# Optimization experiments

Hardware: AMD Instinct MI355X
Metric: run time of the kernel (lower is better)

The kernel has to match this reference:

```python
import jax, jax.numpy as jnp
import numpy as np
from jax import lax

C = 320
GN_GROUPS = 32
EPS = 1e-5


def setup_inputs() -> dict:
    key = jax.random.key(0)
    ks = jax.random.split(key, 5)
    x = jax.random.normal(ks[0], (16, C, 96, 96), dtype=jnp.float32)
    # depthwise 3x3 kernel [C,1,3,3] (OIHW with feature_group_count=C)
    dw_w = jax.random.normal(ks[1], (C, 1, 3, 3), dtype=jnp.float32) * 0.1
    dw_b = jax.random.normal(ks[2], (C,), dtype=jnp.float32) * 0.01
    gn_w = jnp.ones((C,), dtype=jnp.float32)
    gn_b = jnp.zeros((C,), dtype=jnp.float32)
    proj_w = jax.random.normal(ks[3], (C,), dtype=jnp.float32) * 0.001
    proj_b = jnp.full((1,), -4.0, dtype=jnp.float32)
    return {"x": x, "dw_w": dw_w, "dw_b": dw_b, "gn_w": gn_w,
            "gn_b": gn_b, "proj_w": proj_w, "proj_b": proj_b}


def _group_norm(h, gamma, beta):
    # h: [B,C,H,W]; GN over (C//G, H, W) within each of G groups; biased var (torch)
    B, Cc, H, W = h.shape
    hg = h.reshape(B, GN_GROUPS, Cc // GN_GROUPS, H, W)
    mean = jnp.mean(hg, axis=(2, 3, 4), keepdims=True)
    var = jnp.mean(jnp.square(hg - mean), axis=(2, 3, 4), keepdims=True)
    hn = ((hg - mean) * lax.rsqrt(var + EPS)).reshape(B, Cc, H, W)
    return hn * gamma[None, :, None, None] + beta[None, :, None, None]


def reference(x, dw_w, dw_b, gn_w, gn_b, proj_w, proj_b):
    # depthwise 3x3 conv, padding=1
    h = lax.conv_general_dilated(
        x, dw_w, window_strides=(1, 1), padding=((1, 1), (1, 1)),
        dimension_numbers=("NCHW", "OIHW", "NCHW"), feature_group_count=C)
    h = h + dw_b[None, :, None, None]
    h = _group_norm(h, gn_w, gn_b)
    # 1x1 conv C -> 1 == per-pixel channel dot product
    g = jnp.einsum("bchw,c->bhw", h, proj_w) + proj_b[0]
    return jax.nn.sigmoid(g)[:, None, :, :]  # [B,1,H,W]
```

## Files before the change

kernel.cpp:

```cpp
#include <hip/hip_runtime.h>
#include <math.h>

#define HH 96
#define WW 96
#define NPIX (HH*WW)
#define CC 320
#define GG 32
#define CPG 10
#define YT 6
#define TR 16
#define TPB 512

__global__ __launch_bounds__(TPB)
void k_main(const float* __restrict__ x, const float* __restrict__ dw_w,
            const float* __restrict__ dw_b, const float* __restrict__ gn_w,
            const float* __restrict__ proj_w,
            float* __restrict__ P, float* __restrict__ partials) {
  const int bid = blockIdx.x;
  const int yt = bid % YT;
  const int t  = bid / YT;
  const int gr = t & 31;
  const int b  = t >> 5;

  __shared__ float wsm[CPG * 9], ssm[CPG], bsm[CPG];
  const int tid = threadIdx.x;
  if (tid < CPG * 9) wsm[tid] = dw_w[gr * CPG * 9 + tid];
  if (tid < CPG) {
    int c = gr * CPG + tid;
    ssm[tid] = proj_w[c] * gn_w[c];
    bsm[tid] = dw_b[c];
  }
  __syncthreads();

  const int lane = tid & 63;
  const int xcl  = tid & 31;
  const int r    = tid >> 5;
  const bool active = xcl < 24;
  const float mact  = active ? 1.f : 0.f;
  const int xc  = min(xcl, 23);
  const int Y   = yt * TR + r;

  const float mtop = (Y > 0)      ? 1.f : 0.f;
  const float mbot = (Y < HH - 1) ? 1.f : 0.f;
  const int ytop = max(Y - 1, 0);
  const int ybot = min(Y + 1, HH - 1);
  const float mlft = (xcl > 0)  ? 1.f : 0.f;
  const float mrgt = (xcl < 23) ? 1.f : 0.f;
  const int lm1 = (lane >= 1)  ? lane - 1 : lane;
  const int lp1 = (lane <= 62) ? lane + 1 : lane;

  const size_t off_t = (size_t)ytop * WW + xc * 4;
  const size_t off_m = (size_t)Y    * WW + xc * 4;
  const size_t off_b = (size_t)ybot * WW + xc * 4;
  const float* xg = x + ((size_t)(b * CC + gr * CPG)) * NPIX;

  float p0 = 0.f, p1 = 0.f, p2 = 0.f, p3 = 0.f, s1 = 0.f, s2 = 0.f;

  #pragma unroll 1
  for (int cl = 0; cl < CPG; ++cl) {
    const float* img = xg + cl * NPIX;
    float4 vt = *(const float4*)(img + off_t);
    float4 vm = *(const float4*)(img + off_m);
    float4 vb = *(const float4*)(img + off_b);
    vt.x *= mtop; vt.y *= mtop; vt.z *= mtop; vt.w *= mtop;
    vb.x *= mbot; vb.y *= mbot; vb.z *= mbot; vb.w *= mbot;

    float tl = __shfl(vt.w, lm1) * mlft;
    float ml = __shfl(vm.w, lm1) * mlft;
    float bl = __shfl(vb.w, lm1) * mlft;
    float tr_ = __shfl(vt.x, lp1) * mrgt;
    float mr = __shfl(vm.x, lp1) * mrgt;
    float br = __shfl(vb.x, lp1) * mrgt;

    const float* wp = &wsm[cl * 9];
    const float w0 = wp[0], w1 = wp[1], w2 = wp[2];
    const float w3 = wp[3], w4 = wp[4], w5 = wp[5];
    const float w6 = wp[6], w7 = wp[7], w8 = wp[8];

    float u0 = w0*tl   + w1*vt.x + w2*vt.y
             + w3*ml   + w4*vm.x + w5*vm.y
             + w6*bl   + w7*vb.x + w8*vb.y;
    float u1 = w0*vt.x + w1*vt.y + w2*vt.z
             + w3*vm.x + w4*vm.y + w5*vm.z
             + w6*vb.x + w7*vb.y + w8*vb.z;
    float u2 = w0*vt.y + w1*vt.z + w2*vt.w
             + w3*vm.y + w4*vm.z + w5*vm.w
             + w6*vb.y + w7*vb.z + w8*vb.w;
    float u3 = w0*vt.z + w1*vt.w + w2*tr_
             + w3*vm.z + w4*vm.w + w5*mr
             + w6*vb.z + w7*vb.w + w8*br;

    const float sc = ssm[cl], bias = bsm[cl];
    p0 = fmaf(sc, u0, p0);
    p1 = fmaf(sc, u1, p1);
    p2 = fmaf(sc, u2, p2);
    p3 = fmaf(sc, u3, p3);
    float h0 = u0 + bias, h1 = u1 + bias, h2 = u2 + bias, h3 = u3 + bias;
    s1 += mact * ((h0 + h1) + (h2 + h3));
    s2 += mact * (fmaf(h0, h0, h1 * h1) + fmaf(h2, h2, h3 * h3));
  }

  if (active) {
    size_t pidx = ((size_t)(b * GG + gr)) * NPIX + (size_t)Y * WW + xcl * 4;
    *(float4*)&P[pidx] = make_float4(p0, p1, p2, p3);
  }

  #pragma unroll
  for (int off = 32; off; off >>= 1) {
    s1 += __shfl_down(s1, off);
    s2 += __shfl_down(s2, off);
  }
  __shared__ float r1[8], r2[8];
  if ((tid & 63) == 0) { r1[tid >> 6] = s1; r2[tid >> 6] = s2; }
  __syncthreads();
  if (tid == 0) {
    float a = 0.f, q = 0.f;
    #pragma unroll
    for (int i = 0; i < 8; ++i) { a += r1[i]; q += r2[i]; }
    size_t o = (((size_t)(b * GG + gr)) * YT + yt) * 2;
    partials[o]     = a;
    partials[o + 1] = q;
  }
}

__global__ __launch_bounds__(512)
void k_coef(const float* __restrict__ partials, const float* __restrict__ dw_b,
            const float* __restrict__ gn_w, const float* __restrict__ gn_b,
            const float* __restrict__ proj_w, const float* __restrict__ proj_b,
            float* __restrict__ rv, float* __restrict__ D) {
  const int tid = threadIdx.x;
  const int b = tid >> 5, gr = tid & 31;
  float s1 = 0.f, s2 = 0.f;
  #pragma unroll
  for (int t = 0; t < YT; ++t) {
    size_t o = (((size_t)(b * GG + gr)) * YT + t) * 2;
    s1 += partials[o];
    s2 += partials[o + 1];
  }
  const float invN = 1.f / (float)(CPG * NPIX);
  float mean = s1 * invN;
  float var  = s2 * invN - mean * mean;
  float rinv = rsqrtf(var + 1e-5f);
  float K = 0.f, E = 0.f;
  #pragma unroll
  for (int i = 0; i < CPG; ++i) {
    int c = gr * CPG + i;
    float pg = proj_w[c] * gn_w[c];
    K = fmaf(pg, dw_b[c] - mean, K);
    E = fmaf(proj_w[c], gn_b[c], E);
  }
  rv[tid] = rinv;
  float contrib = fmaf(rinv, K, E);
  #pragma unroll
  for (int m = 16; m; m >>= 1) contrib += __shfl_xor(contrib, m, 32);
  if (gr == 0) D[b] = contrib + proj_b[0];
}

__global__ __launch_bounds__(256)
void k_out(const float* __restrict__ P, const float* __restrict__ rv,
           const float* __restrict__ D, float* __restrict__ out) {
  const int b   = blockIdx.x / 9;
  const int blk = blockIdx.x % 9;
  __shared__ float rs[GG];
  __shared__ float Ds;
  if (threadIdx.x < GG) rs[threadIdx.x] = rv[b * GG + threadIdx.x];
  if (threadIdx.x == 0) Ds = D[b];
  __syncthreads();

  const int p = (blk * 256 + threadIdx.x) * 4;
  const float* Pb = P + (size_t)b * GG * NPIX + p;
  float g0 = 0.f, g1 = 0.f, g2 = 0.f, g3 = 0.f;
  #pragma unroll 8
  for (int gr = 0; gr < GG; ++gr) {
    float4 v = *(const float4*)(Pb + (size_t)gr * NPIX);
    float rr = rs[gr];
    g0 = fmaf(rr, v.x, g0);
    g1 = fmaf(rr, v.y, g1);
    g2 = fmaf(rr, v.z, g2);
    g3 = fmaf(rr, v.w, g3);
  }
  const float d = Ds;
  float4 o;
  o.x = 1.f / (1.f + expf(-(g0 + d)));
  o.y = 1.f / (1.f + expf(-(g1 + d)));
  o.z = 1.f / (1.f + expf(-(g2 + d)));
  o.w = 1.f / (1.f + expf(-(g3 + d)));
  *(float4*)&out[(size_t)b * NPIX + p] = o;
}

extern "C" void kernel_launch(void* const* d_in, const int* in_sizes, int n_in,
                              void* d_out, int out_size, void* d_ws, size_t ws_size,
                              hipStream_t stream) {
  const float* x      = (const float*)d_in[0];
  const float* dw_w   = (const float*)d_in[1];
  const float* dw_b   = (const float*)d_in[2];
  const float* gn_w   = (const float*)d_in[3];
  const float* gn_b   = (const float*)d_in[4];
  const float* proj_w = (const float*)d_in[5];
  const float* proj_b = (const float*)d_in[6];
  float* out = (float*)d_out;

  const size_t P_BYTES = (size_t)16 * GG * NPIX * 4;
  float* P        = (float*)d_ws;
  float* partials = (float*)((char*)d_ws + P_BYTES);
  float* rv       = (float*)((char*)d_ws + P_BYTES + 24576);
  float* D        = (float*)((char*)d_ws + P_BYTES + 24576 + 2048);

  hipLaunchKernelGGL(k_main, dim3(16 * GG * YT), dim3(TPB), 0, stream,
                     x, dw_w, dw_b, gn_w, proj_w, P, partials);
  hipLaunchKernelGGL(k_coef, dim3(1), dim3(512), 0, stream,
                     partials, dw_b, gn_w, gn_b, proj_w, proj_b, rv, D);
  hipLaunchKernelGGL(k_out, dim3(16 * 9), dim3(256), 0, stream,
                     P, rv, D, out);
}
```

Measured before the change: 58.36 us.

## Compute two rows per thread with prefetch and fold coef kernel into output kernel

Each thread now computes two output rows, so the four input rows it loads are shared between two stencils and the grid shrinks from 6 to 3 row tiles per group. The next channel's rows are prefetched into registers while the current one is computed. The single-block coefficient kernel is removed; each output block recomputes the group statistics and bias term from the partial sums. This cuts one launch and redundant row loads, at the cost of more registers per thread and some duplicated statistics work in every output block.

New measurement: 52.25 us. -10.5%, faster.

```diff
diff --git a/kernel.cpp b/kernel.cpp
--- a/kernel.cpp
+++ b/kernel.cpp
@@ -7,8 +7,7 @@
 #define CC 320
 #define GG 32
 #define CPG 10
-#define YT 6
-#define TR 16
+#define YT 3
 #define TPB 512
 
 __global__ __launch_bounds__(TPB)
@@ -37,72 +36,87 @@
   const int r    = tid >> 5;
   const bool active = xcl < 24;
   const float mact  = active ? 1.f : 0.f;
-  const int xc  = min(xcl, 23);
-  const int Y   = yt * TR + r;
-
-  const float mtop = (Y > 0)      ? 1.f : 0.f;
-  const float mbot = (Y < HH - 1) ? 1.f : 0.f;
-  const int ytop = max(Y - 1, 0);
-  const int ybot = min(Y + 1, HH - 1);
+  const int xc = min(xcl, 23);
+  const int Y0 = yt * 32 + 2 * r;
+  const int Y1 = Y0 + 1;
+
+  const float ma = (Y0 > 0)      ? 1.f : 0.f;
+  const float md = (Y1 < HH - 1) ? 1.f : 0.f;
+  const int ya = max(Y0 - 1, 0);
+  const int yd = min(Y1 + 1, HH - 1);
   const float mlft = (xcl > 0)  ? 1.f : 0.f;
   const float mrgt = (xcl < 23) ? 1.f : 0.f;
-  const int lm1 = (lane >= 1)  ? lane - 1 : lane;
-  const int lp1 = (lane <= 62) ? lane + 1 : lane;
-
-  const size_t off_t = (size_t)ytop * WW + xc * 4;
-  const size_t off_m = (size_t)Y    * WW + xc * 4;
-  const size_t off_b = (size_t)ybot * WW + xc * 4;
+  const int lm1 = (xcl >= 1) ? lane - 1 : lane;
+  const int lp1 = (xcl < 31) ? lane + 1 : lane;
+
+  const size_t offa = (size_t)ya * WW + xc * 4;
+  const size_t offb = (size_t)Y0 * WW + xc * 4;
+  const size_t offc = (size_t)Y1 * WW + xc * 4;
+  const size_t offd = (size_t)yd * WW + xc * 4;
   const float* xg = x + ((size_t)(b * CC + gr * CPG)) * NPIX;
 
-  float p0 = 0.f, p1 = 0.f, p2 = 0.f, p3 = 0.f, s1 = 0.f, s2 = 0.f;
+  float p0=0.f,p1=0.f,p2=0.f,p3=0.f,p4=0.f,p5=0.f,p6=0.f,p7=0.f;
+  float s1 = 0.f, s2 = 0.f;
+
+  float4 A = *(const float4*)(xg + offa);
+  float4 B = *(const float4*)(xg + offb);
+  float4 C = *(const float4*)(xg + offc);
+  float4 D = *(const float4*)(xg + offd);
 
   #pragma unroll 1
-  for (int cl = 0; cl < CPG; ++cl) {
-    const float* img = xg + cl * NPIX;
-    float4 vt = *(const float4*)(img + off_t);
-    float4 vm = *(const float4*)(img + off_m);
-    float4 vb = *(const float4*)(img + off_b);
-    vt.x *= mtop; vt.y *= mtop; vt.z *= mtop; vt.w *= mtop;
-    vb.x *= mbot; vb.y *= mbot; vb.z *= mbot; vb.w *= mbot;
-
-    float tl = __shfl(vt.w, lm1) * mlft;
-    float ml = __shfl(vm.w, lm1) * mlft;
-    float bl = __shfl(vb.w, lm1) * mlft;
-    float tr_ = __shfl(vt.x, lp1) * mrgt;
-    float mr = __shfl(vm.x, lp1) * mrgt;
-    float br = __shfl(vb.x, lp1) * mrgt;
-
-    const float* wp = &wsm[cl * 9];
+  for (int ch = 0; ch < CPG; ++ch) {
+    const float* nimg = xg + (size_t)min(ch + 1, CPG - 1) * NPIX;
+    float4 nA = *(const float4*)(nimg + offa);
+    float4 nB = *(const float4*)(nimg + offb);
+    float4 nC = *(const float4*)(nimg + offc);
+    float4 nD = *(const float4*)(nimg + offd);
+
+    A.x *= ma; A.y *= ma; A.z *= ma; A.w *= ma;
+    D.x *= md; D.y *= md; D.z *= md; D.w *= md;
+
+    float al = __shfl(A.w, lm1) * mlft;
+    float bl = __shfl(B.w, lm1) * mlft;
+    float cl2 = __shfl(C.w, lm1) * mlft;
+    float dl = __shfl(D.w, lm1) * mlft;
+    float ar = __shfl(A.x, lp1) * mrgt;
+    float br = __shfl(B.x, lp1) * mrgt;
+    float cr = __shfl(C.x, lp1) * mrgt;
+    float dr = __shfl(D.x, lp1) * mrgt;
+
+    const float* wp = &wsm[ch * 9];
     const float w0 = wp[0], w1 = wp[1], w2 = wp[2];
     const float w3 = wp[3], w4 = wp[4], w5 = wp[5];
     const float w6 = wp[6], w7 = wp[7], w8 = wp[8];
 
-    float u0 = w0*tl   + w1*vt.x + w2*vt.y
-             + w3*ml   + w4*vm.x + w5*vm.y
-             + w6*bl   + w7*vb.x + w8*vb.y;
-    float u1 = w0*vt.x + w1*vt.y + w2*vt.z
-             + w3*vm.x + w4*vm.y + w5*vm.z
-             + w6*vb.x + w7*vb.y + w8*vb.z;
-    float u2 = w0*vt.y + w1*vt.z + w2*vt.w
-             + w3*vm.y + w4*vm.z + w5*vm.w
-             + w6*vb.y + w7*vb.z + w8*vb.w;
-    float u3 = w0*vt.z + w1*vt.w + w2*tr_
-             + w3*vm.z + w4*vm.w + w5*mr
-             + w6*vb.z + w7*vb.w + w8*br;
-
-    const float sc = ssm[cl], bias = bsm[cl];
-    p0 = fmaf(sc, u0, p0);
-    p1 = fmaf(sc, u1, p1);
-    p2 = fmaf(sc, u2, p2);
-    p3 = fmaf(sc, u3, p3);
+    float u0 = w0*al  + w1*A.x + w2*A.y + w3*bl  + w4*B.x + w5*B.y + w6*cl2 + w7*C.x + w8*C.y;
+    float u1 = w0*A.x + w1*A.y + w2*A.z + w3*B.x + w4*B.y + w5*B.z + w6*C.x + w7*C.y + w8*C.z;
+    float u2 = w0*A.y + w1*A.z + w2*A.w + w3*B.y + w4*B.z + w5*B.w + w6*C.y + w7*C.z + w8*C.w;
+    float u3 = w0*A.z + w1*A.w + w2*ar  + w3*B.z + w4*B.w + w5*br  + w6*C.z + w7*C.w + w8*cr;
+    float u4 = w0*bl  + w1*B.x + w2*B.y + w3*cl2 + w4*C.x + w5*C.y + w6*dl  + w7*D.x + w8*D.y;
+    float u5 = w0*B.x + w1*B.y + w2*B.z + w3*C.x + w4*C.y + w5*C.z + w6*D.x + w7*D.y + w8*D.z;
+    float u6 = w0*B.y + w1*B.z + w2*B.w + w3*C.y + w4*C.z + w5*C.w + w6*D.y + w7*D.z + w8*D.w;
+    float u7 = w0*B.z + w1*B.w + w2*br  + w3*C.z + w4*C.w + w5*cr  + w6*D.z + w7*D.w + w8*dr;
+
+    const float sc = ssm[ch], bias = bsm[ch];
+    p0 = fmaf(sc, u0, p0); p1 = fmaf(sc, u1, p1);
+    p2 = fmaf(sc, u2, p2); p3 = fmaf(sc, u3, p3);
+    p4 = fmaf(sc, u4, p4); p5 = fmaf(sc, u5, p5);
+    p6 = fmaf(sc, u6, p6); p7 = fmaf(sc, u7, p7);
+
     float h0 = u0 + bias, h1 = u1 + bias, h2 = u2 + bias, h3 = u3 + bias;
-    s1 += mact * ((h0 + h1) + (h2 + h3));
-    s2 += mact * (fmaf(h0, h0, h1 * h1) + fmaf(h2, h2, h3 * h3));
+    float h4 = u4 + bias, h5 = u5 + bias, h6 = u6 + bias, h7 = u7 + bias;
+    s1 += mact * (((h0 + h1) + (h2 + h3)) + ((h4 + h5) + (h6 + h7)));
+    float q0 = fmaf(h0, h0, h1 * h1), q1 = fmaf(h2, h2, h3 * h3);
+    float q2 = fmaf(h4, h4, h5 * h5), q3 = fmaf(h6, h6, h7 * h7);
+    s2 += mact * ((q0 + q1) + (q2 + q3));
+
+    A = nA; B = nB; C = nC; D = nD;
   }
 
   if (active) {
-    size_t pidx = ((size_t)(b * GG + gr)) * NPIX + (size_t)Y * WW + xcl * 4;
-    *(float4*)&P[pidx] = make_float4(p0, p1, p2, p3);
+    size_t base = ((size_t)(b * GG + gr)) * NPIX + (size_t)Y0 * WW + xcl * 4;
+    *(float4*)&P[base]      = make_float4(p0, p1, p2, p3);
+    *(float4*)&P[base + WW] = make_float4(p4, p5, p6, p7);
   }
 
   #pragma unroll
@@ -123,48 +137,43 @@
   }
 }
 
-__global__ __launch_bounds__(512)
-void k_coef(const float* __restrict__ partials, const float* __restrict__ dw_b,
-            const float* __restrict__ gn_w, const float* __restrict__ gn_b,
-            const float* __restrict__ proj_w, const float* __restrict__ proj_b,
-            float* __restrict__ rv, float* __restrict__ D) {
-  const int tid = threadIdx.x;
-  const int b = tid >> 5, gr = tid & 31;
-  float s1 = 0.f, s2 = 0.f;
-  #pragma unroll
-  for (int t = 0; t < YT; ++t) {
-    size_t o = (((size_t)(b * GG + gr)) * YT + t) * 2;
-    s1 += partials[o];
-    s2 += partials[o + 1];
-  }
-  const float invN = 1.f / (float)(CPG * NPIX);
-  float mean = s1 * invN;
-  float var  = s2 * invN - mean * mean;
-  float rinv = rsqrtf(var + 1e-5f);
-  float K = 0.f, E = 0.f;
-  #pragma unroll
-  for (int i = 0; i < CPG; ++i) {
-    int c = gr * CPG + i;
-    float pg = proj_w[c] * gn_w[c];
-    K = fmaf(pg, dw_b[c] - mean, K);
-    E = fmaf(proj_w[c], gn_b[c], E);
-  }
-  rv[tid] = rinv;
-  float contrib = fmaf(rinv, K, E);
-  #pragma unroll
-  for (int m = 16; m; m >>= 1) contrib += __shfl_xor(contrib, m, 32);
-  if (gr == 0) D[b] = contrib + proj_b[0];
-}
-
 __global__ __launch_bounds__(256)
-void k_out(const float* __restrict__ P, const float* __restrict__ rv,
-           const float* __restrict__ D, float* __restrict__ out) {
+void k_out(const float* __restrict__ P, const float* __restrict__ partials,
+           const float* __restrict__ dw_b, const float* __restrict__ gn_w,
+           const float* __restrict__ gn_b, const float* __restrict__ proj_w,
+           const float* __restrict__ proj_b, float* __restrict__ out) {
   const int b   = blockIdx.x / 9;
   const int blk = blockIdx.x % 9;
   __shared__ float rs[GG];
   __shared__ float Ds;
-  if (threadIdx.x < GG) rs[threadIdx.x] = rv[b * GG + threadIdx.x];
-  if (threadIdx.x == 0) Ds = D[b];
+
+  if (threadIdx.x < GG) {
+    const int gr = threadIdx.x;
+    float s1 = 0.f, s2 = 0.f;
+    #pragma unroll
+    for (int t = 0; t < YT; ++t) {
+      size_t o = (((size_t)(b * GG + gr)) * YT + t) * 2;
+      s1 += partials[o];
+      s2 += partials[o + 1];
+    }
+    const float invN = 1.f / (float)(CPG * NPIX);
+    float mean = s1 * invN;
+    float var  = s2 * invN - mean * mean;
+    float rinv = rsqrtf(var + 1e-5f);
+    rs[gr] = rinv;
+    float K = 0.f, E = 0.f;
+    #pragma unroll
+    for (int i = 0; i < CPG; ++i) {
+      int c = gr * CPG + i;
+      float pg = proj_w[c] * gn_w[c];
+      K = fmaf(pg, dw_b[c] - mean, K);
+      E = fmaf(proj_w[c], gn_b[c], E);
+    }
+    float contrib = fmaf(rinv, K, E);
+    #pragma unroll
+    for (int m = 16; m; m >>= 1) contrib += __shfl_xor(contrib, m, 32);
+    if (gr == 0) Ds = contrib + proj_b[0];
+  }
   __syncthreads();
 
   const int p = (blk * 256 + threadIdx.x) * 4;
@@ -203,13 +212,9 @@
   const size_t P_BYTES = (size_t)16 * GG * NPIX * 4;
   float* P        = (float*)d_ws;
   float* partials = (float*)((char*)d_ws + P_BYTES);
-  float* rv       = (float*)((char*)d_ws + P_BYTES + 24576);
-  float* D        = (float*)((char*)d_ws + P_BYTES + 24576 + 2048);
 
   hipLaunchKernelGGL(k_main, dim3(16 * GG * YT), dim3(TPB), 0, stream,
                      x, dw_w, dw_b, gn_w, proj_w, P, partials);
-  hipLaunchKernelGGL(k_coef, dim3(1), dim3(512), 0, stream,
-                     partials, dw_b, gn_w, gn_b, proj_w, proj_b, rv, D);
   hipLaunchKernelGGL(k_out, dim3(16 * 9), dim3(256), 0, stream,
-                     P, rv, D, out);
+                     P, partials, dw_b, gn_w, gn_b, proj_w, proj_b, out);
 }
```
